# Kernel tuning notes

Measured on AMD Instinct MI355X. Metric: run time of the kernel, lower is better.

Reference implementation:

```python
import jax, jax.numpy as jnp
import numpy as np

N = 100000
E = 1600000
EPS = 1e-5

def setup_inputs() -> dict:
    key = jax.random.key(0)
    ks = jax.random.split(key, 10)
    d_in, d_h, d_out = 128, 128, 64
    sc = lambda d: 1.0 / np.sqrt(d)
    return {
        "x": jax.random.normal(ks[0], (N, d_in), jnp.float32),
        "edge_src": jax.random.randint(ks[1], (E,), 0, N, jnp.int32),
        "edge_dst": jax.random.randint(ks[2], (E,), 0, N, jnp.int32),
        "Wr0": jax.random.normal(ks[3], (d_in, d_h), jnp.float32) * sc(d_in),
        "Wn0": jax.random.normal(ks[4], (d_in, d_h), jnp.float32) * sc(d_in),
        "b0": jnp.zeros((d_h,), jnp.float32),
        "g0": jnp.ones((d_h,), jnp.float32),
        "be0": jnp.zeros((d_h,), jnp.float32),
        "Wr1": jax.random.normal(ks[5], (d_h, d_h), jnp.float32) * sc(d_h),
        "Wn1": jax.random.normal(ks[6], (d_h, d_h), jnp.float32) * sc(d_h),
        "b1": jnp.zeros((d_h,), jnp.float32),
        "g1": jnp.ones((d_h,), jnp.float32),
        "be1": jnp.zeros((d_h,), jnp.float32),
        "Wr2": jax.random.normal(ks[7], (d_h, d_out), jnp.float32) * sc(d_h),
        "Wn2": jax.random.normal(ks[8], (d_h, d_out), jnp.float32) * sc(d_h),
        "b2": jnp.zeros((d_out,), jnp.float32),
    }

def _mean_agg(x, src, dst):
    # GraphSAGE mean aggregation: scatter-mean of source features onto dst nodes
    deg = jax.ops.segment_sum(jnp.ones((src.shape[0],), x.dtype), dst, num_segments=N)
    s = jax.ops.segment_sum(x[src], dst, num_segments=N)  # [N, d] gather+scatter
    return s / jnp.maximum(deg, 1.0)[:, None]

def _sage_conv(x, src, dst, Wr, Wn, b):
    return x @ Wr + _mean_agg(x, src, dst) @ Wn + b

def _layernorm(h, g, b):
    mu = h.mean(-1, keepdims=True)
    var = ((h - mu) ** 2).mean(-1, keepdims=True)
    return (h - mu) * jax.lax.rsqrt(var + EPS) * g + b

def reference(x, edge_src, edge_dst, Wr0, Wn0, b0, g0, be0,
              Wr1, Wn1, b1, g1, be1, Wr2, Wn2, b2):
    # layer 0: conv -> dropout(eval=identity) -> LayerNorm -> relu
    h = _sage_conv(x, edge_src, edge_dst, Wr0, Wn0, b0)
    h = jax.nn.relu(_layernorm(h, g0, be0))
    # layer 1
    h = _sage_conv(h, edge_src, edge_dst, Wr1, Wn1, b1)
    h = jax.nn.relu(_layernorm(h, g1, be1))
    # final conv + log_softmax over classes
    h = _sage_conv(h, edge_src, edge_dst, Wr2, Wn2, b2)
    return jax.nn.log_softmax(h, axis=1)
```

## Files before the change

kernel.cpp:

```cpp
#include <hip/hip_runtime.h>
#include <math.h>

#define N_NODES 100000
#define NPAD 100032
#define N_EDGES 1600000
#define EPS 1e-5f
#define NC 256
#define CHUNK 6250
#define NR 98
#define RSZ 1024
#define NRC (NR * NC)
#define EIXL_CAP 1792

typedef __bf16 bf16x8 __attribute__((ext_vector_type(8)));
typedef float f32x4 __attribute__((ext_vector_type(4)));
typedef float f32x2 __attribute__((ext_vector_type(2)));

__device__ inline unsigned short f2bf(float f) {
    unsigned u = __float_as_uint(f);
    unsigned r = u + 0x7fffu + ((u >> 16) & 1u);
    return (unsigned short)(r >> 16);
}
__device__ inline float bflo(unsigned u) { return __uint_as_float(u << 16); }
__device__ inline float bfhi(unsigned u) { return __uint_as_float(u & 0xffff0000u); }
__device__ inline unsigned pack2(float lo, float hi) {
    return (unsigned)f2bf(lo) | ((unsigned)f2bf(hi) << 16);
}
__device__ inline unsigned char f2fp8(float f) {
    return (unsigned char)(__builtin_amdgcn_cvt_pk_fp8_f32(f, f, 0, false) & 0xff);
}

__global__ __launch_bounds__(256) void k_prep(const float* __restrict__ x,
                                              unsigned short* __restrict__ xb,
                                              unsigned* __restrict__ xq8,
                                              const int* __restrict__ dst,
                                              int* __restrict__ cntG) {
    __shared__ int hist[NR];
    int t = threadIdx.x;
    if (blockIdx.x < 12500) {
        int idx = blockIdx.x * 256 + t;
        float4 v = ((const float4*)x)[idx];
        ushort4 o;
        o.x = f2bf(v.x); o.y = f2bf(v.y); o.z = f2bf(v.z); o.w = f2bf(v.w);
        ((ushort4*)xb)[idx] = o;
        int q = __builtin_amdgcn_cvt_pk_fp8_f32(v.x, v.y, 0, false);
        q = __builtin_amdgcn_cvt_pk_fp8_f32(v.z, v.w, q, true);
        xq8[idx] = (unsigned)q;
    } else {
        int c = blockIdx.x - 12500;
        for (int i = t; i < NR; i += 256) hist[i] = 0;
        __syncthreads();
        int base = c * CHUNK;
        for (int i = base + t; i < base + CHUNK; i += 256)
            atomicAdd(&hist[dst[i] >> 10], 1);
        __syncthreads();
        for (int i = t; i < NR; i += 256) cntG[i * NC + c] = hist[i];
    }
}

__global__ __launch_bounds__(256) void k_scanA_prepw(
        int* __restrict__ cntG,
        const float* __restrict__ Wr0, const float* __restrict__ Wn0,
        const float* __restrict__ Wr1, const float* __restrict__ Wn1,
        const float* __restrict__ Wr2, const float* __restrict__ Wn2,
        unsigned short* __restrict__ WT0, unsigned short* __restrict__ WT1,
        unsigned short* __restrict__ WT2) {
    int t = threadIdx.x;
    if (blockIdx.x == 0) {
        __shared__ int ts[256];
        const int PER = NRC / 256;
        int s = 0;
        for (int i = 0; i < PER; ++i) s += cntG[t * PER + i];
        ts[t] = s;
        __syncthreads();
        #pragma unroll
        for (int off = 1; off < 256; off <<= 1) {
            int y = 0;
            if (t >= off) y = ts[t - off];
            __syncthreads();
            if (t >= off) ts[t] += y;
            __syncthreads();
        }
        int run = ts[t] - s;
        for (int i = 0; i < PER; ++i) {
            int v = cntG[t * PER + i];
            cntG[t * PER + i] = run;
            run += v;
        }
    } else {
        int b = blockIdx.x - 1;
        if (b < 256) {
            const float* Wr = (b < 128) ? Wr0 : Wr1;
            const float* Wn = (b < 128) ? Wn0 : Wn1;
            unsigned short* WT = (b < 128) ? WT0 : WT1;
            int idx = (b & 127) * 256 + t;
            int n = idx >> 8;
            int kc = idx & 255;
            float v = (kc < 128) ? Wr[kc * 128 + n] : Wn[(kc - 128) * 128 + n];
            WT[idx] = f2bf(v);
        } else {
            int idx = (b - 256) * 256 + t;
            int n = idx >> 7;
            int k = idx & 127;
            float v = (n < 64) ? Wr2[k * 64 + n] : Wn2[k * 64 + (n - 64)];
            WT2[n * 128 + k] = f2bf(v);
        }
    }
}

__global__ __launch_bounds__(1024) void k_bin(const int* __restrict__ src,
                                              const int* __restrict__ dst,
                                              const int* __restrict__ baseG,
                                              unsigned* __restrict__ bpack) {
    __shared__ int cur[NR];
    int t = threadIdx.x, c = blockIdx.x;
    for (int i = t; i < NR; i += 1024) cur[i] = baseG[i * NC + c];
    __syncthreads();
    int base = c * CHUNK;
    for (int i = base + t; i < base + CHUNK; i += 1024) {
        int d = dst[i];
        unsigned s = (unsigned)src[i];
        int p = atomicAdd(&cur[d >> 10], 1);
        bpack[p] = (s << 10) | (unsigned)(d & 1023);
    }
}

__global__ __launch_bounds__(1024) void k_nodeplace(
        const unsigned* __restrict__ bpack, const int* __restrict__ baseG,
        int* __restrict__ deg, float* __restrict__ invdeg,
        int* __restrict__ rowptr, int* __restrict__ eidx) {
    __shared__ int hist[RSZ];
    __shared__ int cur[RSZ];
    __shared__ int wbase[16];
    int r = blockIdx.x, t = threadIdx.x;
    hist[t] = 0;
    __syncthreads();
    int s0 = baseG[r * NC];
    int s1 = (r == NR - 1) ? N_EDGES : baseG[(r + 1) * NC];
    int nbase = r << 10;
    for (int i = s0 + t; i < s1; i += 1024)
        atomicAdd(&hist[bpack[i] & 1023u], 1);
    __syncthreads();
    int lane = t & 63, wv = t >> 6;
    int d = hist[t];
    int s = d;
    #pragma unroll
    for (int m = 1; m < 64; m <<= 1) {
        int y = __shfl_up(s, m);
        if (lane >= m) s += y;
    }
    if (lane == 63) wbase[wv] = s;
    __syncthreads();
    if (t < 16) {
        int v = wbase[t];
        int sv = v;
        #pragma unroll
        for (int m = 1; m < 16; m <<= 1) {
            int y = __shfl_up(sv, m);
            if (t >= m) sv += y;
        }
        wbase[t] = sv - v;
    }
    __syncthreads();
    int p = s0 + wbase[wv] + s - d;
    cur[t] = p;
    int n = nbase + t;
    if (n < N_NODES) {
        rowptr[n] = p;
        deg[n] = d;
        invdeg[n] = 1.0f / fmaxf((float)d, 1.0f);
    }
    __syncthreads();
    for (int i = s0 + t; i < s1; i += 1024) {
        unsigned bp = bpack[i];
        int pp = atomicAdd(&cur[bp & 1023u], 1);
        eidx[pp] = (int)(bp >> 10);
    }
}

__global__ __launch_bounds__(512, 6) void k_gemm_ln(
        const unsigned short* __restrict__ hb,
        const uint4* __restrict__ hq4,
        const int* __restrict__ eidx, const int* __restrict__ rowptr,
        const int* __restrict__ deg, const float* __restrict__ invdeg,
        const unsigned short* __restrict__ WT,
        const float* __restrict__ b, const float* __restrict__ g,
        const float* __restrict__ be, unsigned short* __restrict__ outb,
        unsigned char* __restrict__ outq8) {
    __shared__ unsigned short hl[64][136];
    __shared__ unsigned short al[64][136];
    __shared__ unsigned short bt[128][40];
    __shared__ float p1[2][64], p2[2][64];
    __shared__ int eixl[EIXL_CAP];

    const int tid = threadIdx.x;
    const int lane = tid & 63;
    const int w = tid >> 6;
    const int quad = lane >> 4;
    const int l15 = lane & 15;
    const int rt = w >> 1;
    const int ch = w & 1;
    const int row0 = blockIdx.x * 64;

    #pragma unroll
    for (int t = 0; t < 2; ++t) {
        int idx = tid + t * 512;
        int r = idx >> 4;
        int c8 = idx & 15;
        *(float4*)&hl[r][c8 * 8] = ((const float4*)hb)[(size_t)(row0 + r) * 16 + c8];
    }

    int e0 = rowptr[row0];
    int e1 = (row0 + 64 < N_NODES) ? rowptr[row0 + 64] : N_EDGES;
    int nE = e1 - e0;
    int staged = nE < EIXL_CAP ? nE : EIXL_CAP;
    for (int i = tid; i < staged; i += 512) eixl[i] = eidx[e0 + i];
    __syncthreads();

    {
        int r = tid >> 3;
        int l = tid & 7;
        int node = row0 + r;
        uint4 o0 = {0, 0, 0, 0}, o1 = {0, 0, 0, 0};
        if (node < N_NODES) {
            int start = rowptr[node];
            int cnt = deg[node];
            int rel = start - e0;
            f32x2 a[8];
            #pragma unroll
            for (int i = 0; i < 8; ++i) a[i] = (f32x2)0.0f;
            auto accum = [&](uint4 u) {
                a[0] += __builtin_amdgcn_cvt_pk_f32_fp8((int)u.x, false);
                a[1] += __builtin_amdgcn_cvt_pk_f32_fp8((int)u.x, true);
                a[2] += __builtin_amdgcn_cvt_pk_f32_fp8((int)u.y, false);
                a[3] += __builtin_amdgcn_cvt_pk_f32_fp8((int)u.y, true);
                a[4] += __builtin_amdgcn_cvt_pk_f32_fp8((int)u.z, false);
                a[5] += __builtin_amdgcn_cvt_pk_f32_fp8((int)u.z, true);
                a[6] += __builtin_amdgcn_cvt_pk_f32_fp8((int)u.w, false);
                a[7] += __builtin_amdgcn_cvt_pk_f32_fp8((int)u.w, true);
            };
            if (rel + cnt <= staged) {
                int nb = cnt >> 3;
                for (int bq = 0; bq < nb; ++bq) {
                    int jb = rel + bq * 8;
                    int i0 = eixl[jb + 0], i1 = eixl[jb + 1];
                    int i2 = eixl[jb + 2], i3 = eixl[jb + 3];
                    int i4 = eixl[jb + 4], i5 = eixl[jb + 5];
                    int i6 = eixl[jb + 6], i7 = eixl[jb + 7];
                    uint4 u0 = hq4[(unsigned)(i0 * 8 + l)];
                    uint4 u1 = hq4[(unsigned)(i1 * 8 + l)];
                    uint4 u2 = hq4[(unsigned)(i2 * 8 + l)];
                    uint4 u3 = hq4[(unsigned)(i3 * 8 + l)];
                    uint4 u4 = hq4[(unsigned)(i4 * 8 + l)];
                    uint4 u5 = hq4[(unsigned)(i5 * 8 + l)];
                    uint4 u6 = hq4[(unsigned)(i6 * 8 + l)];
                    uint4 u7 = hq4[(unsigned)(i7 * 8 + l)];
                    accum(u0); accum(u1); accum(u2); accum(u3);
                    accum(u4); accum(u5); accum(u6); accum(u7);
                }
                int j = nb << 3;
                int rem = cnt - j;
                #pragma unroll
                for (int k = 0; k < 8; ++k) {
                    if (k < rem) {
                        uint4 u = hq4[(unsigned)(eixl[rel + j + k] * 8 + l)];
                        accum(u);
                    }
                }
            } else {
                int j = 0;
                for (; j + 4 <= cnt; j += 4) {
                    int s0 = eidx[start + j];
                    int s1 = eidx[start + j + 1];
                    int s2 = eidx[start + j + 2];
                    int s3 = eidx[start + j + 3];
                    uint4 u0 = hq4[(unsigned)(s0 * 8 + l)];
                    uint4 u1 = hq4[(unsigned)(s1 * 8 + l)];
                    uint4 u2 = hq4[(unsigned)(s2 * 8 + l)];
                    uint4 u3 = hq4[(unsigned)(s3 * 8 + l)];
                    accum(u0); accum(u1); accum(u2); accum(u3);
                }
                for (; j < cnt; ++j) {
                    uint4 u = hq4[(unsigned)(eidx[start + j] * 8 + l)];
                    accum(u);
                }
            }
            float id = invdeg[node];
            o0.x = pack2(a[0].x * id, a[0].y * id);
            o0.y = pack2(a[1].x * id, a[1].y * id);
            o0.z = pack2(a[2].x * id, a[2].y * id);
            o0.w = pack2(a[3].x * id, a[3].y * id);
            o1.x = pack2(a[4].x * id, a[4].y * id);
            o1.y = pack2(a[5].x * id, a[5].y * id);
            o1.z = pack2(a[6].x * id, a[6].y * id);
            o1.w = pack2(a[7].x * id, a[7].y * id);
        }
        *(uint4*)&al[r][l * 16] = o0;
        *(uint4*)&al[r][l * 16 + 8] = o1;
    }

    f32x4 acc[4];
    #pragma unroll
    for (int t = 0; t < 4; ++t)
        #pragma unroll
        for (int r = 0; r < 4; ++r) acc[t][r] = 0.0f;

    #pragma unroll
    for (int kt = 0; kt < 8; ++kt) {
        __syncthreads();
        {
            int n = tid >> 2;
            int c = tid & 3;
            *(float4*)&bt[n][c * 8] = ((const float4*)WT)[n * 32 + kt * 4 + c];
        }
        __syncthreads();
        const int ck = kt * 32;
        const unsigned short* ap = (ck < 128)
            ? &hl[rt * 16 + l15][ck + quad * 8]
            : &al[rt * 16 + l15][ck - 128 + quad * 8];
        bf16x8 a = *(const bf16x8*)ap;
        #pragma unroll
        for (int t = 0; t < 4; ++t) {
            bf16x8 bb = *(const bf16x8*)&bt[ch * 64 + t * 16 + l15][quad * 8];
            acc[t] = __builtin_amdgcn_mfma_f32_16x16x32_bf16(a, bb, acc[t], 0, 0, 0);
        }
    }

    float bcol[4], gc[4], bec[4];
    #pragma unroll
    for (int t = 0; t < 4; ++t) {
        int col = ch * 64 + t * 16 + l15;
        bcol[t] = b[col]; gc[t] = g[col]; bec[t] = be[col];
    }
    float v[4][4];
    float s1[4], s2[4];
    #pragma unroll
    for (int r = 0; r < 4; ++r) { s1[r] = 0.0f; s2[r] = 0.0f; }
    #pragma unroll
    for (int t = 0; t < 4; ++t)
        #pragma unroll
        for (int r = 0; r < 4; ++r) {
            float x = acc[t][r] + bcol[t];
            v[t][r] = x;
            s1[r] += x;
            s2[r] += x * x;
        }
    #pragma unroll
    for (int m = 1; m <= 8; m <<= 1)
        #pragma unroll
        for (int r = 0; r < 4; ++r) {
            s1[r] += __shfl_xor(s1[r], m);
            s2[r] += __shfl_xor(s2[r], m);
        }
    if (l15 == 0) {
        #pragma unroll
        for (int r = 0; r < 4; ++r) {
            int rl = rt * 16 + quad * 4 + r;
            p1[ch][rl] = s1[r];
            p2[ch][rl] = s2[r];
        }
    }
    __syncthreads();
    #pragma unroll
    for (int r = 0; r < 4; ++r) {
        int rl = rt * 16 + quad * 4 + r;
        float S1 = p1[0][rl] + p1[1][rl];
        float S2 = p2[0][rl] + p2[1][rl];
        float mean = S1 * (1.0f / 128.0f);
        float var = S2 * (1.0f / 128.0f) - mean * mean;
        float rstd = rsqrtf(var + EPS);
        #pragma unroll
        for (int t = 0; t < 4; ++t) {
            int col = ch * 64 + t * 16 + l15;
            float o = fmaxf((v[t][r] - mean) * rstd * gc[t] + bec[t], 0.0f);
            outb[(size_t)(row0 + rl) * 128 + col] = f2bf(o);
            if (outq8) outq8[(size_t)(row0 + rl) * 128 + col] = f2fp8(o);
        }
    }
}

__global__ __launch_bounds__(512) void k_gemm2(
        const unsigned short* __restrict__ hb, const unsigned short* __restrict__ WT,
        const float* __restrict__ b2, unsigned short* __restrict__ zb16,
        unsigned char* __restrict__ yq8) {
    __shared__ unsigned short hl[64][136];
    __shared__ unsigned short bt[128][136];

    const int tid = threadIdx.x;
    const int lane = tid & 63;
    const int w = tid >> 6;
    const int quad = lane >> 4;
    const int l15 = lane & 15;
    const int rt = w >> 1;
    const int ch = w & 1;
    const int row0 = blockIdx.x * 64;

    #pragma unroll
    for (int t = 0; t < 2; ++t) {
        int idx = tid + t * 512;
        int r = idx >> 4;
        int c8 = idx & 15;
        *(float4*)&hl[r][c8 * 8] = ((const float4*)hb)[(size_t)(row0 + r) * 16 + c8];
    }
    #pragma unroll
    for (int t = 0; t < 4; ++t) {
        int idx = tid + t * 512;
        int n = idx >> 4;
        int c8 = idx & 15;
        *(float4*)&bt[n][c8 * 8] = ((const float4*)WT)[n * 16 + c8];
    }
    __syncthreads();

    f32x4 acc[4];
    #pragma unroll
    for (int t = 0; t < 4; ++t)
        #pragma unroll
        for (int r = 0; r < 4; ++r) acc[t][r] = 0.0f;

    #pragma unroll
    for (int ks = 0; ks < 4; ++ks) {
        bf16x8 a = *(const bf16x8*)&hl[rt * 16 + l15][ks * 32 + quad * 8];
        #pragma unroll
        for (int t = 0; t < 4; ++t) {
            bf16x8 bb = *(const bf16x8*)&bt[ch * 64 + t * 16 + l15][ks * 32 + quad * 8];
            acc[t] = __builtin_amdgcn_mfma_f32_16x16x32_bf16(a, bb, acc[t], 0, 0, 0);
        }
    }

    if (ch == 0) {
        #pragma unroll
        for (int t = 0; t < 4; ++t) {
            int col = t * 16 + l15;
            float bc = b2[col];
            #pragma unroll
            for (int r = 0; r < 4; ++r) {
                int rl = rt * 16 + quad * 4 + r;
                zb16[(size_t)(row0 + rl) * 64 + col] = f2bf(acc[t][r] + bc);
            }
        }
    } else {
        #pragma unroll
        for (int t = 0; t < 4; ++t) {
            int col = t * 16 + l15;
            #pragma unroll
            for (int r = 0; r < 4; ++r) {
                int rl = rt * 16 + quad * 4 + r;
                yq8[(size_t)(row0 + rl) * 64 + col] = f2fp8(acc[t][r]);
            }
        }
    }
}

__global__ __launch_bounds__(256) void k_l2g(const uint4* __restrict__ yq4,
                                             const unsigned short* __restrict__ zb16,
                                             const int* __restrict__ eidx,
                                             const int* __restrict__ rowptr,
                                             const int* __restrict__ deg,
                                             const float* __restrict__ invdeg,
                                             float* __restrict__ out) {
    __shared__ int eixl[EIXL_CAP];
    int node0 = blockIdx.x * 64;
    int e0 = rowptr[node0];
    int e1 = (node0 + 64 < N_NODES) ? rowptr[node0 + 64] : N_EDGES;
    int nE = e1 - e0;
    int staged = nE < EIXL_CAP ? nE : EIXL_CAP;
    for (int i = threadIdx.x; i < staged; i += 256) eixl[i] = eidx[e0 + i];
    __syncthreads();

    int node = node0 + (threadIdx.x >> 2);
    if (node >= N_NODES) return;
    int l = threadIdx.x & 3;
    int start = rowptr[node];
    int cnt = deg[node];
    int rel = start - e0;
    f32x2 a[8];
    #pragma unroll
    for (int i = 0; i < 8; ++i) a[i] = (f32x2)0.0f;

    auto accum = [&](uint4 u) {
        a[0] += __builtin_amdgcn_cvt_pk_f32_fp8((int)u.x, false);
        a[1] += __builtin_amdgcn_cvt_pk_f32_fp8((int)u.x, true);
        a[2] += __builtin_amdgcn_cvt_pk_f32_fp8((int)u.y, false);
        a[3] += __builtin_amdgcn_cvt_pk_f32_fp8((int)u.y, true);
        a[4] += __builtin_amdgcn_cvt_pk_f32_fp8((int)u.z, false);
        a[5] += __builtin_amdgcn_cvt_pk_f32_fp8((int)u.z, true);
        a[6] += __builtin_amdgcn_cvt_pk_f32_fp8((int)u.w, false);
        a[7] += __builtin_amdgcn_cvt_pk_f32_fp8((int)u.w, true);
    };

    if (rel + cnt <= staged) {
        int nb = cnt >> 3;
        for (int bq = 0; bq < nb; ++bq) {
            int jb = rel + bq * 8;
            int i0 = eixl[jb + 0], i1 = eixl[jb + 1];
            int i2 = eixl[jb + 2], i3 = eixl[jb + 3];
            int i4 = eixl[jb + 4], i5 = eixl[jb + 5];
            int i6 = eixl[jb + 6], i7 = eixl[jb + 7];
            uint4 u0 = yq4[(unsigned)(i0 * 4 + l)];
            uint4 u1 = yq4[(unsigned)(i1 * 4 + l)];
            uint4 u2 = yq4[(unsigned)(i2 * 4 + l)];
            uint4 u3 = yq4[(unsigned)(i3 * 4 + l)];
            uint4 u4 = yq4[(unsigned)(i4 * 4 + l)];
            uint4 u5 = yq4[(unsigned)(i5 * 4 + l)];
            uint4 u6 = yq4[(unsigned)(i6 * 4 + l)];
            uint4 u7 = yq4[(unsigned)(i7 * 4 + l)];
            accum(u0); accum(u1); accum(u2); accum(u3);
            accum(u4); accum(u5); accum(u6); accum(u7);
        }
        int j = nb << 3;
        int rem = cnt - j;
        #pragma unroll
        for (int k = 0; k < 8; ++k) {
            if (k < rem) {
                uint4 u = yq4[(unsigned)(eixl[rel + j + k] * 4 + l)];
                accum(u);
            }
        }
    } else {
        int j = 0;
        for (; j + 4 <= cnt; j += 4) {
            int s0 = eidx[start + j];
            int s1 = eidx[start + j + 1];
            int s2 = eidx[start + j + 2];
            int s3 = eidx[start + j + 3];
            uint4 u0 = yq4[(unsigned)(s0 * 4 + l)];
            uint4 u1 = yq4[(unsigned)(s1 * 4 + l)];
            uint4 u2 = yq4[(unsigned)(s2 * 4 + l)];
            uint4 u3 = yq4[(unsigned)(s3 * 4 + l)];
            accum(u0); accum(u1); accum(u2); accum(u3);
        }
        for (; j < cnt; ++j) {
            uint4 u = yq4[(unsigned)(eidx[start + j] * 4 + l)];
            accum(u);
        }
    }

    float id = invdeg[node];
    uint4 z0 = ((const uint4*)zb16)[(size_t)node * 8 + l * 2];
    uint4 z1 = ((const uint4*)zb16)[(size_t)node * 8 + l * 2 + 1];
    float v[16];
    v[0]  = bflo(z0.x) + a[0].x * id; v[1]  = bfhi(z0.x) + a[0].y * id;
    v[2]  = bflo(z0.y) + a[1].x * id; v[3]  = bfhi(z0.y) + a[1].y * id;
    v[4]  = bflo(z0.z) + a[2].x * id; v[5]  = bfhi(z0.z) + a[2].y * id;
    v[6]  = bflo(z0.w) + a[3].x * id; v[7]  = bfhi(z0.w) + a[3].y * id;
    v[8]  = bflo(z1.x) + a[4].x * id; v[9]  = bfhi(z1.x) + a[4].y * id;
    v[10] = bflo(z1.y) + a[5].x * id; v[11] = bfhi(z1.y) + a[5].y * id;
    v[12] = bflo(z1.z) + a[6].x * id; v[13] = bfhi(z1.z) + a[6].y * id;
    v[14] = bflo(z1.w) + a[7].x * id; v[15] = bfhi(z1.w) + a[7].y * id;

    float m = v[0];
    #pragma unroll
    for (int i = 1; i < 16; ++i) m = fmaxf(m, v[i]);
    m = fmaxf(m, __shfl_xor(m, 1));
    m = fmaxf(m, __shfl_xor(m, 2));
    float s = 0.0f;
    #pragma unroll
    for (int i = 0; i < 16; ++i) s += __expf(v[i] - m);
    s += __shfl_xor(s, 1);
    s += __shfl_xor(s, 2);
    float L = m + logf(s);
    #pragma unroll
    for (int k = 0; k < 4; ++k) {
        float4 o;
        o.x = v[4 * k] - L; o.y = v[4 * k + 1] - L;
        o.z = v[4 * k + 2] - L; o.w = v[4 * k + 3] - L;
        ((float4*)out)[(size_t)node * 16 + l * 4 + k] = o;
    }
}

extern "C" void kernel_launch(void* const* d_in, const int* in_sizes, int n_in,
                              void* d_out, int out_size, void* d_ws, size_t ws_size,
                              hipStream_t stream) {
    const float* x   = (const float*)d_in[0];
    const int* esrc  = (const int*)d_in[1];
    const int* edst  = (const int*)d_in[2];
    const float* Wr0 = (const float*)d_in[3];
    const float* Wn0 = (const float*)d_in[4];
    const float* b0  = (const float*)d_in[5];
    const float* g0  = (const float*)d_in[6];
    const float* be0 = (const float*)d_in[7];
    const float* Wr1 = (const float*)d_in[8];
    const float* Wn1 = (const float*)d_in[9];
    const float* b1  = (const float*)d_in[10];
    const float* g1  = (const float*)d_in[11];
    const float* be1 = (const float*)d_in[12];
    const float* Wr2 = (const float*)d_in[13];
    const float* Wn2 = (const float*)d_in[14];
    const float* b2  = (const float*)d_in[15];
    float* out = (float*)d_out;

    char* p = (char*)d_ws;
    auto alloc = [&](size_t bytes) {
        void* r = (void*)p;
        p += (bytes + 255) & ~(size_t)255;
        return r;
    };
    int*   deg    = (int*)  alloc(N_NODES * 4);
    float* invdeg = (float*)alloc(N_NODES * 4);
    int*   rowptr = (int*)  alloc(N_NODES * 4);
    int*   cntG   = (int*)  alloc(NRC * 4);
    unsigned* bpack = (unsigned*)alloc((size_t)N_EDGES * 4);
    int*   eidx   = (int*)  alloc((size_t)N_EDGES * 4);
    unsigned short* xb   = (unsigned short*)alloc((size_t)NPAD * 128 * 2);
    unsigned short* h1   = (unsigned short*)alloc((size_t)NPAD * 128 * 2);
    unsigned*       xq8  = (unsigned*)      alloc((size_t)N_NODES * 128);
    unsigned char*  h1q8 = (unsigned char*) alloc((size_t)NPAD * 128);
    unsigned short* zb16 = (unsigned short*)alloc((size_t)NPAD * 64 * 2);
    unsigned char*  yq8  = (unsigned char*) alloc((size_t)NPAD * 64);
    unsigned short* WT0  = (unsigned short*)alloc(128 * 256 * 2);
    unsigned short* WT1  = (unsigned short*)alloc(128 * 256 * 2);
    unsigned short* WT2  = (unsigned short*)alloc(128 * 128 * 2);

    k_prep<<<12500 + NC, 256, 0, stream>>>(x, xb, xq8, edst, cntG);
    k_scanA_prepw<<<321, 256, 0, stream>>>(cntG, Wr0, Wn0, Wr1, Wn1, Wr2, Wn2,
                                           WT0, WT1, WT2);
    k_bin<<<NC, 1024, 0, stream>>>(esrc, edst, cntG, bpack);
    k_nodeplace<<<NR, 1024, 0, stream>>>(bpack, cntG, deg, invdeg, rowptr, eidx);

    k_gemm_ln<<<NPAD / 64, 512, 0, stream>>>(xb, (const uint4*)xq8, eidx, rowptr,
                                             deg, invdeg, WT0, b0, g0, be0, h1, h1q8);

    k_gemm_ln<<<NPAD / 64, 512, 0, stream>>>(h1, (const uint4*)h1q8, eidx, rowptr,
                                             deg, invdeg, WT1, b1, g1, be1, xb,
                                             (unsigned char*)nullptr);

    k_gemm2<<<NPAD / 64, 512, 0, stream>>>(xb, WT2, b2, zb16, yq8);
    k_l2g<<<(N_NODES + 63) / 64, 256, 0, stream>>>((const uint4*)yq8, zb16, eidx, rowptr, deg, invdeg, out);
}
```

Baseline: 329.3 us.

## Load self-feature MFMA operands into registers and raise occupancy of fused gemm kernel

Removes the hl shared-memory tile and instead loads each wave's self-feature A fragments directly from global into registers, cutting LDS usage by about 17 KB per block. Launch bounds rise from 6 to 8 waves per SIMD target, and the neighbor-gather loop is unrolled by 4 instead of 8 to reduce register pressure. The trade-off is less memory-level parallelism per thread in the gather and possible register spilling under the tighter bound, while the extra occupancy is meant to hide gather latency.

New measurement: 320.1 us, median of 2. -2.8%, faster.

```diff
diff --git a/kernel.cpp b/kernel.cpp
--- a/kernel.cpp
+++ b/kernel.cpp
@@ -178,7 +178,7 @@
     }
 }
 
-__global__ __launch_bounds__(512, 6) void k_gemm_ln(
+__global__ __launch_bounds__(512, 8) void k_gemm_ln(
         const unsigned short* __restrict__ hb,
         const uint4* __restrict__ hq4,
         const int* __restrict__ eidx, const int* __restrict__ rowptr,
@@ -187,7 +187,6 @@
         const float* __restrict__ b, const float* __restrict__ g,
         const float* __restrict__ be, unsigned short* __restrict__ outb,
         unsigned char* __restrict__ outq8) {
-    __shared__ unsigned short hl[64][136];
     __shared__ unsigned short al[64][136];
     __shared__ unsigned short bt[128][40];
     __shared__ float p1[2][64], p2[2][64];
@@ -202,12 +201,12 @@
     const int ch = w & 1;
     const int row0 = blockIdx.x * 64;
 
-    #pragma unroll
-    for (int t = 0; t < 2; ++t) {
-        int idx = tid + t * 512;
-        int r = idx >> 4;
-        int c8 = idx & 15;
-        *(float4*)&hl[r][c8 * 8] = ((const float4*)hb)[(size_t)(row0 + r) * 16 + c8];
+    bf16x8 selfA[4];
+    {
+        const unsigned short* base = hb + (size_t)(row0 + rt * 16 + l15) * 128 + quad * 8;
+        #pragma unroll
+        for (int kt = 0; kt < 4; ++kt)
+            selfA[kt] = *(const bf16x8*)(base + kt * 32);
     }
 
     int e0 = rowptr[row0];
@@ -240,32 +239,19 @@
                 a[7] += __builtin_amdgcn_cvt_pk_f32_fp8((int)u.w, true);
             };
             if (rel + cnt <= staged) {
-                int nb = cnt >> 3;
-                for (int bq = 0; bq < nb; ++bq) {
-                    int jb = rel + bq * 8;
-                    int i0 = eixl[jb + 0], i1 = eixl[jb + 1];
-                    int i2 = eixl[jb + 2], i3 = eixl[jb + 3];
-                    int i4 = eixl[jb + 4], i5 = eixl[jb + 5];
-                    int i6 = eixl[jb + 6], i7 = eixl[jb + 7];
+                int j = 0;
+                for (; j + 4 <= cnt; j += 4) {
+                    int i0 = eixl[rel + j + 0], i1 = eixl[rel + j + 1];
+                    int i2 = eixl[rel + j + 2], i3 = eixl[rel + j + 3];
                     uint4 u0 = hq4[(unsigned)(i0 * 8 + l)];
                     uint4 u1 = hq4[(unsigned)(i1 * 8 + l)];
                     uint4 u2 = hq4[(unsigned)(i2 * 8 + l)];
                     uint4 u3 = hq4[(unsigned)(i3 * 8 + l)];
-                    uint4 u4 = hq4[(unsigned)(i4 * 8 + l)];
-                    uint4 u5 = hq4[(unsigned)(i5 * 8 + l)];
-                    uint4 u6 = hq4[(unsigned)(i6 * 8 + l)];
-                    uint4 u7 = hq4[(unsigned)(i7 * 8 + l)];
                     accum(u0); accum(u1); accum(u2); accum(u3);
-                    accum(u4); accum(u5); accum(u6); accum(u7);
                 }
-                int j = nb << 3;
-                int rem = cnt - j;
-                #pragma unroll
-                for (int k = 0; k < 8; ++k) {
-                    if (k < rem) {
-                        uint4 u = hq4[(unsigned)(eixl[rel + j + k] * 8 + l)];
-                        accum(u);
-                    }
+                for (; j < cnt; ++j) {
+                    uint4 u = hq4[(unsigned)(eixl[rel + j] * 8 + l)];
+                    accum(u);
                 }
             } else {
                 int j = 0;
@@ -314,11 +300,9 @@
             *(float4*)&bt[n][c * 8] = ((const float4*)WT)[n * 32 + kt * 4 + c];
         }
         __syncthreads();
-        const int ck = kt * 32;
-        const unsigned short* ap = (ck < 128)
-            ? &hl[rt * 16 + l15][ck + quad * 8]
-            : &al[rt * 16 + l15][ck - 128 + quad * 8];
-        bf16x8 a = *(const bf16x8*)ap;
+        bf16x8 a = (kt < 4)
+            ? selfA[kt]
+            : *(const bf16x8*)&al[rt * 16 + l15][(kt - 4) * 32 + quad * 8];
         #pragma unroll
         for (int t = 0; t < 4; ++t) {
             bf16x8 bb = *(const bf16x8*)&bt[ch * 64 + t * 16 + l15][quad * 8];
```
